# Kernel optimization log

Hardware: AMD Instinct MI355X
Metric: run time of the kernel (lower is better)

Reference implementation:

```python
import jax, jax.numpy as jnp
import numpy as np

B, DIM, H, W = 1, 256, 64, 64
NUM_HEADS = 8
N_GROUPS = 4
KK = 9                      # ksizes[blk_ids=0]
KV_H, KV_W = 64, 64         # kv_size[blk_ids=0]
NGC = DIM // N_GROUPS       # n_group_channels = 64
NHC = DIM // NUM_HEADS      # n_head_channels = 32
NGH = NUM_HEADS // N_GROUPS # n_group_heads = 2
OFFSET_RANGE_FACTOR = 2.0
SCALE = NHC ** -0.5
LN_EPS = 1e-5


def setup_inputs() -> dict:
    key = jax.random.key(0)
    ks = jax.random.split(key, 10)
    def n(k, shape, std=0.02):
        return jax.random.normal(k, shape, jnp.float32) * std
    return {
        "x": jax.random.normal(ks[0], (B, DIM, H, W), jnp.float32),
        "wq": n(ks[1], (DIM, DIM)), "bq": jnp.zeros((DIM,), jnp.float32),
        "wk": n(ks[2], (DIM, DIM)), "bk": jnp.zeros((DIM,), jnp.float32),
        "wv": n(ks[3], (DIM, DIM)), "bv": jnp.zeros((DIM,), jnp.float32),
        "w_off_dw": n(ks[4], (NGC, 1, KK, KK)), "b_off_dw": jnp.zeros((NGC,), jnp.float32),
        "ln_g": jnp.ones((NGC,), jnp.float32), "ln_b": jnp.zeros((NGC,), jnp.float32),
        "w_off_pw": n(ks[5], (2, NGC)),
        "rpe_table": n(ks[6], (NUM_HEADS, 2 * KV_H - 1, 2 * KV_W - 1), 0.01),
        "w_out": n(ks[7], (DIM, DIM)), "b_out": jnp.zeros((DIM,), jnp.float32),
    }


def conv1x1(x, w, b=None):
    # x: [B,C,H,W], w: [O,C]
    y = jnp.einsum('bchw,oc->bohw', x, w)
    if b is not None:
        y = y + b[None, :, None, None]
    return y


def grid_sample_bilinear(inp, grid):
    # Faithful F.grid_sample(mode='bilinear', align_corners=True, padding_mode='zeros').
    # inp: [N,C,Hi,Wi], grid: [N,Hg,Wg,2] with (x,y) in [-1,1].
    N, C, Hi, Wi = inp.shape
    gx = (grid[..., 0] + 1.0) * 0.5 * (Wi - 1)
    gy = (grid[..., 1] + 1.0) * 0.5 * (Hi - 1)
    x0 = jnp.floor(gx)
    y0 = jnp.floor(gy)
    gather_b = jax.vmap(lambda im, iy, ix: im[:, iy, ix])  # -> [N,C,Hg,Wg]
    out = jnp.zeros((N, C) + grid.shape[1:3], inp.dtype)
    for dy in (0.0, 1.0):
        for dx in (0.0, 1.0):
            ix = x0 + dx
            iy = y0 + dy
            wgt = (1.0 - jnp.abs(gx - ix)) * (1.0 - jnp.abs(gy - iy))
            valid = (ix >= 0) & (ix <= Wi - 1) & (iy >= 0) & (iy <= Hi - 1)
            ixc = jnp.clip(ix, 0, Wi - 1).astype(jnp.int32)
            iyc = jnp.clip(iy, 0, Hi - 1).astype(jnp.int32)
            out = out + gather_b(inp, iyc, ixc) * (wgt * valid)[:, None]
    return out


def ref_points(Hk, Wk, n):
    # normalized (y, x) reference grid, matching _get_ref_points
    ry = (jnp.arange(Hk, dtype=jnp.float32) + 0.5) / Hk * 2.0 - 1.0
    rx = (jnp.arange(Wk, dtype=jnp.float32) + 0.5) / Wk * 2.0 - 1.0
    ref = jnp.stack(jnp.meshgrid(ry, rx, indexing='ij'), -1)  # [Hk,Wk,2]
    return jnp.broadcast_to(ref[None], (n, Hk, Wk, 2))


def reference(x, wq, bq, wk, bk, wv, bv, w_off_dw, b_off_dw, ln_g, ln_b,
              w_off_pw, rpe_table, w_out, b_out):
    Bx, C, Hx, Wx = x.shape
    q = conv1x1(x, wq, bq)
    q_off = q.reshape(Bx * N_GROUPS, NGC, Hx, Wx)

    # conv_offset: depthwise conv -> LayerNorm(channels) -> GELU -> 1x1 conv (no bias)
    o = jax.lax.conv_general_dilated(
        q_off, w_off_dw, window_strides=(1, 1),
        padding=[(KK // 2, KK // 2), (KK // 2, KK // 2)],
        feature_group_count=NGC,
        dimension_numbers=('NCHW', 'OIHW', 'NCHW'))
    o = o + b_off_dw[None, :, None, None]
    mu = o.mean(1, keepdims=True)
    var = o.var(1, keepdims=True)
    o = (o - mu) / jnp.sqrt(var + LN_EPS) * ln_g[None, :, None, None] + ln_b[None, :, None, None]
    o = jax.nn.gelu(o, approximate=False)
    offset = jnp.einsum('bchw,oc->bohw', o, w_off_pw)  # [B*g, 2, Hk, Wk]

    Hk, Wk = offset.shape[2], offset.shape[3]
    n_sample = Hk * Wk
    off_range = jnp.array([1.0 / Hk, 1.0 / Wk], jnp.float32).reshape(1, 2, 1, 1)
    offset = jnp.tanh(offset) * off_range * OFFSET_RANGE_FACTOR
    offset = offset.transpose(0, 2, 3, 1)  # [B*g, Hk, Wk, 2] (y, x)

    pos = offset + ref_points(Hk, Wk, Bx * N_GROUPS)

    x_g = x.reshape(Bx * N_GROUPS, NGC, Hx, Wx)
    x_sampled = grid_sample_bilinear(x_g, pos[..., ::-1])  # grid is (x, y)
    x_sampled = x_sampled.reshape(Bx, C, 1, n_sample)

    qf = q.reshape(Bx * NUM_HEADS, NHC, Hx * Wx)
    k = conv1x1(x_sampled, wk, bk).reshape(Bx * NUM_HEADS, NHC, n_sample)
    v = conv1x1(x_sampled, wv, bv).reshape(Bx * NUM_HEADS, NHC, n_sample)

    attn = jnp.einsum('bcm,bcn->bmn', qf, k) * SCALE  # [B*h, HW, n_sample]

    # RPE bias via bilinear sampling of rpe_table at displacement grid
    q_grid = ref_points(Hx, Wx, Bx * N_GROUPS)
    disp = (q_grid.reshape(Bx * N_GROUPS, Hx * Wx, 1, 2)
            - pos.reshape(Bx * N_GROUPS, 1, n_sample, 2)) * 0.5
    rpe = jnp.broadcast_to(rpe_table[None], (Bx,) + rpe_table.shape)
    rpe = rpe.reshape(Bx * N_GROUPS, NGH, 2 * Hx - 1, 2 * Wx - 1)
    attn_bias = grid_sample_bilinear(rpe, disp[..., ::-1])
    attn_bias = attn_bias.reshape(Bx * NUM_HEADS, Hx * Wx, n_sample)

    attn = jax.nn.softmax(attn + attn_bias, axis=2)
    out = jnp.einsum('bmn,bcn->bcm', attn, v).reshape(Bx, C, Hx, Wx)
    return conv1x1(out, w_out, b_out)
```

## Files before the change

### kernel.cpp

```cpp
#include <hip/hip_runtime.h>
#include <hip/hip_bf16.h>
#include <math.h>

#define HW 4096
#define SCALE 0.17677669529663687f
#define LOG2E 1.4426950408889634f

typedef __attribute__((ext_vector_type(8))) short short8;
typedef __attribute__((ext_vector_type(4))) float f32x4;
typedef __attribute__((ext_vector_type(4), aligned(4))) float f32x4u;
typedef __attribute__((ext_vector_type(4))) unsigned int u32x4;
typedef __attribute__((ext_vector_type(2))) unsigned int u32x2;

static __device__ __forceinline__ unsigned short bf16b(float f) {
  __hip_bfloat16 h = __float2bfloat16(f);
  return *reinterpret_cast<unsigned short*>(&h);
}

__global__ __launch_bounds__(256) void gemm256(const float* __restrict__ W,
                                               const float* __restrict__ bias,
                                               const float* __restrict__ X,
                                               float* __restrict__ Yf,
                                               unsigned short* __restrict__ Yt,
                                               unsigned short* __restrict__ Yv,
                                               float sc) {
  int tid = threadIdx.x;
  int o0 = (blockIdx.x >> 3) * 8;
  int p = (blockIdx.x & 7) * 512 + tid * 2;
  const float* Wb = W + o0 * 256;
  float ax[8], ay[8];
  #pragma unroll
  for (int i = 0; i < 8; ++i) { ax[i] = 0.f; ay[i] = 0.f; }
  #pragma unroll 4
  for (int c = 0; c < 256; ++c) {
    float2 xv = *(const float2*)(X + c * HW + p);
    #pragma unroll
    for (int i = 0; i < 8; ++i) {
      float wv = Wb[i * 256 + c];
      ax[i] += wv * xv.x;
      ay[i] += wv * xv.y;
    }
  }
  float rx[8], ry[8];
  #pragma unroll
  for (int i = 0; i < 8; ++i) {
    float b = bias[o0 + i];
    rx[i] = ax[i] + b;
    ry[i] = ay[i] + b;
  }
  if (Yf) {
    #pragma unroll
    for (int i = 0; i < 8; ++i) {
      float2 st = {rx[i], ry[i]};
      *(float2*)(Yf + (size_t)(o0 + i) * HW + p) = st;
    }
  }
  if (Yt) {
    int h = o0 >> 5, c0 = o0 & 31;
    u32x4 pk0, pk1;
    #pragma unroll
    for (int j = 0; j < 4; ++j) {
      pk0[j] = (unsigned int)bf16b(rx[2 * j] * sc) | ((unsigned int)bf16b(rx[2 * j + 1] * sc) << 16);
      pk1[j] = (unsigned int)bf16b(ry[2 * j] * sc) | ((unsigned int)bf16b(ry[2 * j + 1] * sc) << 16);
    }
    *(u32x4*)(Yt + ((size_t)(h * HW + p) * 32 + c0)) = pk0;
    *(u32x4*)(Yt + ((size_t)(h * HW + p + 1) * 32 + c0)) = pk1;
  }
  if (Yv) {
    #pragma unroll
    for (int i = 0; i < 8; ++i) {
      unsigned int pk = (unsigned int)bf16b(rx[i]) | ((unsigned int)bf16b(ry[i]) << 16);
      *(unsigned int*)(Yv + (size_t)(o0 + i) * HW + p) = pk;
    }
  }
}

__global__ __launch_bounds__(256) void dwconv_kernel(const float* __restrict__ q,
                                                     const float* __restrict__ wdw,
                                                     const float* __restrict__ bdw,
                                                     float* __restrict__ o) {
  int x = threadIdx.x & 63;
  int w = threadIdx.x >> 6;
  int bid = blockIdx.x;
  int half = bid & 1; int c = (bid >> 1) & 63; int g = bid >> 7;
  int y0 = half * 32 + w * 8;
  const float* qc = q + (g * 64 + c) * HW;
  const float* wc = wdw + c * 81;
  float b = bdw[c];
  float acc[8];
  #pragma unroll
  for (int i = 0; i < 8; ++i) acc[i] = b;
  #pragma unroll
  for (int r = 0; r < 16; ++r) {
    int yy = y0 - 4 + r;
    bool rowok = (unsigned)yy <= 63u;
    int yc = min(max(yy, 0), 63);
    float v[9];
    #pragma unroll
    for (int kx = 0; kx < 9; ++kx) {
      int xx = x + kx - 4;
      bool ok = rowok && ((unsigned)xx <= 63u);
      int xc = min(max(xx, 0), 63);
      float lv = qc[yc * 64 + xc];
      v[kx] = ok ? lv : 0.f;
    }
    #pragma unroll
    for (int oy = 0; oy < 8; ++oy) {
      int ky = r - oy;
      if (ky < 0 || ky > 8) continue;
      #pragma unroll
      for (int kx = 0; kx < 9; ++kx)
        acc[oy] += wc[ky * 9 + kx] * v[kx];
    }
  }
  #pragma unroll
  for (int oy = 0; oy < 8; ++oy)
    o[(g * 64 + c) * HW + (y0 + oy) * 64 + x] = acc[oy];
}

__global__ __launch_bounds__(256) void ln_offset_kernel(const float* __restrict__ o,
                                                        const float* __restrict__ ln_g,
                                                        const float* __restrict__ ln_b,
                                                        const float* __restrict__ wpw,
                                                        float* __restrict__ pos,
                                                        float* __restrict__ cxy) {
  int wave = threadIdx.x >> 6;
  int c = threadIdx.x & 63;
  int bid = blockIdx.x;
  int xc = bid & 15; int y = (bid >> 4) & 63; int g = bid >> 10;
  int x = xc * 4 + wave;
  int p = y * 64 + x;
  float v = o[(g * 64 + c) * HW + p];
  float s = v, s2 = v * v;
  #pragma unroll
  for (int m = 32; m; m >>= 1) { s += __shfl_xor(s, m); s2 += __shfl_xor(s2, m); }
  float mu = s * (1.f / 64.f);
  float var = s2 * (1.f / 64.f) - mu * mu;
  float nv = (v - mu) * rsqrtf(var + 1e-5f) * ln_g[c] + ln_b[c];
  nv = 0.5f * nv * (1.f + erff(nv * 0.70710678118654752f));
  float t0 = wpw[c] * nv, t1 = wpw[64 + c] * nv;
  #pragma unroll
  for (int m = 32; m; m >>= 1) { t0 += __shfl_xor(t0, m); t1 += __shfl_xor(t1, m); }
  if (c == 0) {
    float offy = tanhf(t0) * (2.0f / 64.0f);
    float offx = tanhf(t1) * (2.0f / 64.0f);
    float py = offy + (y + 0.5f) * (2.f / 64.f) - 1.f;
    float px = offx + (x + 0.5f) * (2.f / 64.f) - 1.f;
    pos[(g * HW + p) * 2 + 0] = py;
    pos[(g * HW + p) * 2 + 1] = px;
    cxy[(g * HW + p) * 2 + 0] = 64.0f - 31.5f * px;
    cxy[(g * HW + p) * 2 + 1] = 64.0f - 31.5f * py;
  }
}

__global__ __launch_bounds__(256) void sample_kernel(const float* __restrict__ x,
                                                     const float* __restrict__ pos,
                                                     float* __restrict__ xs) {
  int bid = blockIdx.x;
  int cc = bid & 3; int nt = (bid >> 2) & 15; int g = bid >> 6;
  int n = nt * 256 + threadIdx.x;
  float py = pos[(g * HW + n) * 2 + 0];
  float px = pos[(g * HW + n) * 2 + 1];
  float gx = (px + 1.f) * 31.5f;
  float gy = (py + 1.f) * 31.5f;
  float xf = floorf(gx), yf = floorf(gy);
  int xi = (int)xf, yi = (int)yf;
  float fx = gx - xf, fy = gy - yf;
  int x0c = min(max(xi, 0), 63), x1c = min(max(xi + 1, 0), 63);
  int y0c = min(max(yi, 0), 63), y1c = min(max(yi + 1, 0), 63);
  float wx0 = ((unsigned)xi <= 63u) ? (1.f - fx) : 0.f;
  float wx1 = ((unsigned)(xi + 1) <= 63u) ? fx : 0.f;
  float wy0 = ((unsigned)yi <= 63u) ? (1.f - fy) : 0.f;
  float wy1 = ((unsigned)(yi + 1) <= 63u) ? fy : 0.f;
  #pragma unroll 4
  for (int ci = 0; ci < 16; ++ci) {
    int c = cc * 16 + ci;
    const float* xp = x + (g * 64 + c) * HW;
    float vsum = wy0 * (wx0 * xp[y0c * 64 + x0c] + wx1 * xp[y0c * 64 + x1c]) +
                 wy1 * (wx0 * xp[y1c * 64 + x0c] + wx1 * xp[y1c * 64 + x1c]);
    xs[(g * 64 + c) * HW + n] = vsum;
  }
}

__global__ __launch_bounds__(256) void build_rpe2_kernel(const float* __restrict__ rpe,
                                                         float* __restrict__ tab2) {
  int idx = blockIdx.x * 256 + threadIdx.x;
  if (idx >= 8 * 16641) return;
  int h = idx / 16641; int r = idx - h * 16641;
  int y = r / 129, x = r - y * 129;
  float v0 = 0.f, v1 = 0.f;
  if (x >= 1 && x <= 127) {
    if (y >= 1 && y <= 127) v0 = rpe[(h * 127 + (y - 1)) * 127 + (x - 1)] * LOG2E;
    if (y + 1 >= 1 && y + 1 <= 127) v1 = rpe[(h * 127 + y) * 127 + (x - 1)] * LOG2E;
  }
  float2 v = {v0 - 32.0f, v1 - 32.0f};
  *(float2*)(tab2 + (size_t)idx * 2) = v;
}

__global__ __launch_bounds__(256, 6) void attn_kernel(const unsigned short* __restrict__ qt,
                                                      const unsigned short* __restrict__ kt,
                                                      const unsigned short* __restrict__ vbuf,
                                                      const float* __restrict__ cxy,
                                                      const float* __restrict__ tpad2,
                                                      float* __restrict__ att) {
  __shared__ __align__(16) unsigned int P_pack[4][16][20];
  __shared__ float red_l[4][16];
  __shared__ float red_acc[4][32][16];

  int tid = threadIdx.x;
  int w = tid >> 6;
  int l = tid & 63;
  int lm = l & 15;
  int lg = l >> 4;
  int h = blockIdx.x >> 8;
  int mt = blockIdx.x & 255;
  int m0 = mt * 16;
  int m = m0 + lm;
  int xm = m & 63, ym = m >> 6;
  float ex = (xm + 0.5f) * (63.0f / 64.0f) - 31.5f;
  float ey = (ym + 0.5f) * (63.0f / 64.0f) - 31.5f;
  const char* tabb = (const char*)(tpad2 + (size_t)h * 33282);
  const float* cbase = cxy + (size_t)(h >> 1) * HW * 2;

  short8 qf = *(const short8*)(qt + ((size_t)(h * HW + m) * 32 + 8 * lg));

  f32x4 oA = {0.f, 0.f, 0.f, 0.f};
  f32x4 oB = {0.f, 0.f, 0.f, 0.f};
  float l_lane = 0.f;

  float2 ccv[8];
  #pragma unroll
  for (int i = 0; i < 8; ++i) {
    int nl = 16 * (i >> 2) + 4 * lg + (i & 3);
    ccv[i] = *(const float2*)(cbase + (size_t)(w * 32 + nl) * 2);
  }

  for (int it = 0; it < 32; ++it) {
    int n0 = (it * 4 + w) * 32;
    short8 ka = *(const short8*)(kt + ((size_t)(h * HW + n0 + lm) * 32 + 8 * lg));
    short8 kb = *(const short8*)(kt + ((size_t)(h * HW + n0 + 16 + lm) * 32 + 8 * lg));
    f32x4 z = {0.f, 0.f, 0.f, 0.f};
    f32x4 s0 = __builtin_amdgcn_mfma_f32_16x16x32_bf16(ka, qf, z, 0, 0, 0);
    f32x4 s1 = __builtin_amdgcn_mfma_f32_16x16x32_bf16(kb, qf, z, 0, 0, 0);
    short8 va = *(const short8*)(vbuf + ((size_t)(h * 32 + lm) * HW + n0 + 8 * lg));
    short8 vb = *(const short8*)(vbuf + ((size_t)(h * 32 + 16 + lm) * HW + n0 + 8 * lg));

    int n0n = (((it + 1) & 31) * 4 + w) * 32;
    float2 ccn[8];
    #pragma unroll
    for (int i = 0; i < 8; ++i) {
      int nl = 16 * (i >> 2) + 4 * lg + (i & 3);
      ccn[i] = *(const float2*)(cbase + (size_t)(n0n + nl) * 2);
    }

    float p[8];
    #pragma unroll
    for (int i = 0; i < 8; ++i) {
      float gx = ex + ccv[i].x, gy = ey + ccv[i].y;
      float xf = floorf(gx), yf = floorf(gy);
      float fx = gx - xf, fy = gy - yf;
      int xi = (int)xf, yi = (int)yf;
      unsigned off = (unsigned)(yi * 1032 + (xi << 3));
      f32x4u tv = *(const f32x4u*)(tabb + off);
      float ly0 = tv[0] + fy * (tv[1] - tv[0]);
      float ly1 = tv[2] + fy * (tv[3] - tv[2]);
      float qk = (i < 4) ? s0[i & 3] : s1[i & 3];
      p[i] = __builtin_amdgcn_exp2f(qk + (ly0 + fx * (ly1 - ly0)));
      l_lane += p[i];
    }
    unsigned int w0, w1, w2, w3;
    asm("v_cvt_pk_bf16_f32 %0, %1, %2" : "=v"(w0) : "v"(p[0]), "v"(p[1]));
    asm("v_cvt_pk_bf16_f32 %0, %1, %2" : "=v"(w1) : "v"(p[2]), "v"(p[3]));
    asm("v_cvt_pk_bf16_f32 %0, %1, %2" : "=v"(w2) : "v"(p[4]), "v"(p[5]));
    asm("v_cvt_pk_bf16_f32 %0, %1, %2" : "=v"(w3) : "v"(p[6]), "v"(p[7]));
    u32x2 wa = {w0, w1}, wb = {w2, w3};
    *(u32x2*)&P_pack[w][lm][2 * lg] = wa;
    *(u32x2*)&P_pack[w][lm][8 + 2 * lg] = wb;
    u32x4 pw = *(u32x4*)&P_pack[w][lm][4 * lg];
    union { u32x4 u; short8 s; } cv; cv.u = pw;
    oA = __builtin_amdgcn_mfma_f32_16x16x32_bf16(va, cv.s, oA, 0, 0, 0);
    oB = __builtin_amdgcn_mfma_f32_16x16x32_bf16(vb, cv.s, oB, 0, 0, 0);
    #pragma unroll
    for (int i = 0; i < 8; ++i) ccv[i] = ccn[i];
  }

  l_lane += __shfl_xor(l_lane, 16);
  l_lane += __shfl_xor(l_lane, 32);
  if (lg == 0) red_l[w][lm] = l_lane;
  #pragma unroll
  for (int r = 0; r < 4; ++r) {
    red_acc[w][4 * lg + r][lm] = oA[r];
    red_acc[w][16 + 4 * lg + r][lm] = oB[r];
  }
  __syncthreads();
  #pragma unroll
  for (int rep = 0; rep < 2; ++rep) {
    int idx = tid + rep * 256;
    int cl = idx >> 4, mm = idx & 15;
    float lsum = 0.f, osum = 0.f;
    #pragma unroll
    for (int ww = 0; ww < 4; ++ww) {
      lsum += red_l[ww][mm];
      osum += red_acc[ww][cl][mm];
    }
    att[(size_t)(h * 32 + cl) * HW + m0 + mm] = osum / lsum;
  }
}

extern "C" void kernel_launch(void* const* d_in, const int* in_sizes, int n_in,
                              void* d_out, int out_size, void* d_ws, size_t ws_size,
                              hipStream_t stream) {
  const float* x    = (const float*)d_in[0];
  const float* wq   = (const float*)d_in[1];
  const float* bq   = (const float*)d_in[2];
  const float* wk   = (const float*)d_in[3];
  const float* bk   = (const float*)d_in[4];
  const float* wv   = (const float*)d_in[5];
  const float* bv   = (const float*)d_in[6];
  const float* wdw  = (const float*)d_in[7];
  const float* bdw  = (const float*)d_in[8];
  const float* lng  = (const float*)d_in[9];
  const float* lnb  = (const float*)d_in[10];
  const float* wpw  = (const float*)d_in[11];
  const float* rpe  = (const float*)d_in[12];
  const float* wout = (const float*)d_in[13];
  const float* bout = (const float*)d_in[14];
  float* out = (float*)d_out;

  float* ws = (float*)d_ws;
  float* q_f32 = ws;
  float* o_f32 = ws + (1 << 20);
  unsigned short* qt  = (unsigned short*)(ws + (2 << 20));
  unsigned short* ktp = (unsigned short*)(ws + ((2 << 20) + (1 << 19)));
  unsigned short* vbp = (unsigned short*)(ws + (3 << 20));
  float* pos  = ws + ((3 << 20) + (1 << 19));
  float* cxy  = pos + 32768;
  float* tab2 = cxy + 32768;

  gemm256<<<256, 256, 0, stream>>>(wq, bq, x, q_f32, qt, nullptr, SCALE * LOG2E);
  build_rpe2_kernel<<<521, 256, 0, stream>>>(rpe, tab2);
  dwconv_kernel<<<512, 256, 0, stream>>>(q_f32, wdw, bdw, o_f32);
  ln_offset_kernel<<<4096, 256, 0, stream>>>(o_f32, lng, lnb, wpw, pos, cxy);
  sample_kernel<<<256, 256, 0, stream>>>(x, pos, q_f32);
  gemm256<<<256, 256, 0, stream>>>(wk, bk, q_f32, nullptr, ktp, nullptr, 1.0f);
  gemm256<<<256, 256, 0, stream>>>(wv, bv, q_f32, nullptr, nullptr, vbp, 1.0f);
  attn_kernel<<<2048, 256, 0, stream>>>(qt, ktp, vbp, cxy, tab2, o_f32);
  gemm256<<<256, 256, 0, stream>>>(wout, bout, o_f32, out, nullptr, nullptr, 1.0f);
}
```

Baseline: 328.7 us.

## Software-pipeline attention loop: prefetch K/V, RPE bias one iteration ahead

Restructures the attention inner loop into a deeper software pipeline. K/V fragments for the next tile are loaded during the current iteration, and the RPE table gathers for the next tile are issued before the current softmax/PV step, with the bilinear interpolation done after the MFMAs. Coordinate loads are prefetched two iterations ahead. Launch bounds drop from 6 to 3 blocks per SM to make room for the extra live registers. The inline-asm bf16 pack is replaced with a library conversion. This trades occupancy for instruction-level latency hiding, and the new bf16 conversion may cost more instructions.

Measured after the change: 319.2 us. -2.9%, faster.

```diff
diff --git a/kernel.cpp b/kernel.cpp
--- a/kernel.cpp
+++ b/kernel.cpp
@@ -197,7 +197,7 @@
   *(float2*)(tab2 + (size_t)idx * 2) = v;
 }
 
-__global__ __launch_bounds__(256, 6) void attn_kernel(const unsigned short* __restrict__ qt,
+__global__ __launch_bounds__(256, 3) void attn_kernel(const unsigned short* __restrict__ qt,
                                                       const unsigned short* __restrict__ kt,
                                                       const unsigned short* __restrict__ vbuf,
                                                       const float* __restrict__ cxy,
@@ -228,51 +228,86 @@
   f32x4 oB = {0.f, 0.f, 0.f, 0.f};
   float l_lane = 0.f;
 
+  float bias[8];
   float2 ccv[8];
-  #pragma unroll
-  for (int i = 0; i < 8; ++i) {
-    int nl = 16 * (i >> 2) + 4 * lg + (i & 3);
-    ccv[i] = *(const float2*)(cbase + (size_t)(w * 32 + nl) * 2);
-  }
-
+  short8 ka, kb, va, vb;
+
+  {
+    float2 cc0[8];
+    #pragma unroll
+    for (int i = 0; i < 8; ++i) {
+      int nl = 16 * (i >> 2) + 4 * lg + (i & 3);
+      cc0[i] = *(const float2*)(cbase + (size_t)(w * 32 + nl) * 2);
+    }
+    int n0 = w * 32;
+    ka = *(const short8*)(kt + ((size_t)(h * HW + n0 + lm) * 32 + 8 * lg));
+    kb = *(const short8*)(kt + ((size_t)(h * HW + n0 + 16 + lm) * 32 + 8 * lg));
+    va = *(const short8*)(vbuf + ((size_t)(h * 32 + lm) * HW + n0 + 8 * lg));
+    vb = *(const short8*)(vbuf + ((size_t)(h * 32 + 16 + lm) * HW + n0 + 8 * lg));
+    f32x4u tv[8];
+    float fxs[8], fys[8];
+    #pragma unroll
+    for (int i = 0; i < 8; ++i) {
+      float gx = ex + cc0[i].x, gy = ey + cc0[i].y;
+      float xf = floorf(gx), yf = floorf(gy);
+      fxs[i] = gx - xf; fys[i] = gy - yf;
+      unsigned off = (unsigned)((int)yf * 1032 + ((int)xf << 3));
+      tv[i] = *(const f32x4u*)(tabb + off);
+    }
+    #pragma unroll
+    for (int i = 0; i < 8; ++i) {
+      int nl = 16 * (i >> 2) + 4 * lg + (i & 3);
+      ccv[i] = *(const float2*)(cbase + (size_t)(128 + w * 32 + nl) * 2);
+    }
+    #pragma unroll
+    for (int i = 0; i < 8; ++i) {
+      float ly0 = tv[i][0] + fys[i] * (tv[i][1] - tv[i][0]);
+      float ly1 = tv[i][2] + fys[i] * (tv[i][3] - tv[i][2]);
+      bias[i] = ly0 + fxs[i] * (ly1 - ly0);
+    }
+  }
+
+  #pragma unroll 2
   for (int it = 0; it < 32; ++it) {
-    int n0 = (it * 4 + w) * 32;
-    short8 ka = *(const short8*)(kt + ((size_t)(h * HW + n0 + lm) * 32 + 8 * lg));
-    short8 kb = *(const short8*)(kt + ((size_t)(h * HW + n0 + 16 + lm) * 32 + 8 * lg));
     f32x4 z = {0.f, 0.f, 0.f, 0.f};
     f32x4 s0 = __builtin_amdgcn_mfma_f32_16x16x32_bf16(ka, qf, z, 0, 0, 0);
     f32x4 s1 = __builtin_amdgcn_mfma_f32_16x16x32_bf16(kb, qf, z, 0, 0, 0);
-    short8 va = *(const short8*)(vbuf + ((size_t)(h * 32 + lm) * HW + n0 + 8 * lg));
-    short8 vb = *(const short8*)(vbuf + ((size_t)(h * 32 + 16 + lm) * HW + n0 + 8 * lg));
-
-    int n0n = (((it + 1) & 31) * 4 + w) * 32;
-    float2 ccn[8];
-    #pragma unroll
-    for (int i = 0; i < 8; ++i) {
-      int nl = 16 * (i >> 2) + 4 * lg + (i & 3);
-      ccn[i] = *(const float2*)(cbase + (size_t)(n0n + nl) * 2);
-    }
-
-    float p[8];
+
+    int n0n = ((it + 1) & 31) * 128 + w * 32;
+    short8 kan = *(const short8*)(kt + ((size_t)(h * HW + n0n + lm) * 32 + 8 * lg));
+    short8 kbn = *(const short8*)(kt + ((size_t)(h * HW + n0n + 16 + lm) * 32 + 8 * lg));
+    short8 van = *(const short8*)(vbuf + ((size_t)(h * 32 + lm) * HW + n0n + 8 * lg));
+    short8 vbn = *(const short8*)(vbuf + ((size_t)(h * 32 + 16 + lm) * HW + n0n + 8 * lg));
+
+    f32x4u tv[8];
+    float fxs[8], fys[8];
     #pragma unroll
     for (int i = 0; i < 8; ++i) {
       float gx = ex + ccv[i].x, gy = ey + ccv[i].y;
       float xf = floorf(gx), yf = floorf(gy);
-      float fx = gx - xf, fy = gy - yf;
-      int xi = (int)xf, yi = (int)yf;
-      unsigned off = (unsigned)(yi * 1032 + (xi << 3));
-      f32x4u tv = *(const f32x4u*)(tabb + off);
-      float ly0 = tv[0] + fy * (tv[1] - tv[0]);
-      float ly1 = tv[2] + fy * (tv[3] - tv[2]);
+      fxs[i] = gx - xf; fys[i] = gy - yf;
+      unsigned off = (unsigned)((int)yf * 1032 + ((int)xf << 3));
+      tv[i] = *(const f32x4u*)(tabb + off);
+    }
+    int n0n2 = ((it + 2) & 31) * 128 + w * 32;
+    float2 ccn[8];
+    #pragma unroll
+    for (int i = 0; i < 8; ++i) {
+      int nl = 16 * (i >> 2) + 4 * lg + (i & 3);
+      ccn[i] = *(const float2*)(cbase + (size_t)(n0n2 + nl) * 2);
+    }
+
+    float p[8];
+    #pragma unroll
+    for (int i = 0; i < 8; ++i) {
       float qk = (i < 4) ? s0[i & 3] : s1[i & 3];
-      p[i] = __builtin_amdgcn_exp2f(qk + (ly0 + fx * (ly1 - ly0)));
-      l_lane += p[i];
-    }
-    unsigned int w0, w1, w2, w3;
-    asm("v_cvt_pk_bf16_f32 %0, %1, %2" : "=v"(w0) : "v"(p[0]), "v"(p[1]));
-    asm("v_cvt_pk_bf16_f32 %0, %1, %2" : "=v"(w1) : "v"(p[2]), "v"(p[3]));
-    asm("v_cvt_pk_bf16_f32 %0, %1, %2" : "=v"(w2) : "v"(p[4]), "v"(p[5]));
-    asm("v_cvt_pk_bf16_f32 %0, %1, %2" : "=v"(w3) : "v"(p[6]), "v"(p[7]));
+      p[i] = __builtin_amdgcn_exp2f(qk + bias[i]);
+    }
+    l_lane += ((p[0] + p[1]) + (p[2] + p[3])) + ((p[4] + p[5]) + (p[6] + p[7]));
+    unsigned int w0 = (unsigned int)bf16b(p[0]) | ((unsigned int)bf16b(p[1]) << 16);
+    unsigned int w1 = (unsigned int)bf16b(p[2]) | ((unsigned int)bf16b(p[3]) << 16);
+    unsigned int w2 = (unsigned int)bf16b(p[4]) | ((unsigned int)bf16b(p[5]) << 16);
+    unsigned int w3 = (unsigned int)bf16b(p[6]) | ((unsigned int)bf16b(p[7]) << 16);
     u32x2 wa = {w0, w1}, wb = {w2, w3};
     *(u32x2*)&P_pack[w][lm][2 * lg] = wa;
     *(u32x2*)&P_pack[w][lm][8 + 2 * lg] = wb;
@@ -280,6 +315,14 @@
     union { u32x4 u; short8 s; } cv; cv.u = pw;
     oA = __builtin_amdgcn_mfma_f32_16x16x32_bf16(va, cv.s, oA, 0, 0, 0);
     oB = __builtin_amdgcn_mfma_f32_16x16x32_bf16(vb, cv.s, oB, 0, 0, 0);
+
+    #pragma unroll
+    for (int i = 0; i < 8; ++i) {
+      float ly0 = tv[i][0] + fys[i] * (tv[i][1] - tv[i][0]);
+      float ly1 = tv[i][2] + fys[i] * (tv[i][3] - tv[i][2]);
+      bias[i] = ly0 + fxs[i] * (ly1 - ly0);
+    }
+    ka = kan; kb = kbn; va = van; vb = vbn;
     #pragma unroll
     for (int i = 0; i < 8; ++i) ccv[i] = ccn[i];
   }
```
